# Kernel optimization log

Hardware: AMD Instinct MI355X
Metric: run time of the kernel (lower is better)

## Reference

```python
import jax, jax.numpy as jnp
import numpy as np

B, NP, NG = 4, 8192, 8192

def setup_inputs() -> dict:
    key = jax.random.key(0)
    k1, k2, k3 = jax.random.split(key, 3)
    pr_pts = jax.random.normal(k1, (B, NP, 3), dtype=jnp.float32)
    gt_pts = jax.random.normal(k2, (B, NG, 3), dtype=jnp.float32)
    gt_valid = jax.random.randint(k3, (B, NG), 0, 2) > 0
    return {"pr_pts": pr_pts, "gt_pts": gt_pts, "gt_valid": gt_valid}

def _sq_dists(a, b):
    # a: [B,N,3], b: [B,M,3] -> squared pairwise distances [B,N,M]
    a2 = jnp.sum(a * a, -1)  # [B,N]
    b2 = jnp.sum(b * b, -1)  # [B,M]
    ab = jnp.einsum('bnd,bmd->bnm', a, b)
    return a2[:, :, None] + b2[:, None, :] - 2.0 * ab

def reference(pr_pts, gt_pts, gt_valid):
    # Bidirectional Chamfer distance with gt validity mask.
    d2 = _sq_dists(pr_pts, gt_pts)  # [B,Np,Ng]
    # accuracy: for each predicted point, min squared dist to a VALID gt point
    d2_masked = jnp.where(gt_valid[:, None, :], d2, jnp.inf)
    acc_b = jnp.mean(jnp.min(d2_masked, axis=-1), axis=-1)  # [B]
    # completeness: for each valid gt point, min squared dist to any pred point
    min_over_pr = jnp.min(d2, axis=1)  # [B,Ng]
    valid_f = gt_valid.astype(min_over_pr.dtype)
    com_b = jnp.sum(min_over_pr * valid_f, axis=-1) / jnp.maximum(jnp.sum(valid_f, axis=-1), 1.0)
    loss_acc = jnp.mean(acc_b)
    loss_com = jnp.mean(com_b)
    loss_cd = loss_acc + loss_com
    # Sum((loss_acc,None),(loss_com,None),(loss_cd,None)) with scalar losses -> acc+com+cd
    return loss_acc + loss_com + loss_cd
```

## Files before the change

kernel.cpp:

```cpp
#include <hip/hip_runtime.h>

#define BB 4
#define NN 8192

typedef _Float16 f16;
typedef _Float16 f16x8 __attribute__((ext_vector_type(8)));
typedef float f32x16 __attribute__((ext_vector_type(16)));

#define SZ_PACK (BB * NN * 16)
#define OFF_PART_BYTES (4 * SZ_PACK * 2)
#define OFF_RES_BYTES (OFF_PART_BYTES + 16 * NN * 4)

__global__ __launch_bounds__(256) void k_init(
    const float* __restrict__ pr, const float* __restrict__ gt,
    const int* __restrict__ valid,
    f16* __restrict__ APR, f16* __restrict__ BGT,
    f16* __restrict__ AGT, f16* __restrict__ BPR,
    float* __restrict__ res) {
  int i = blockIdx.x * 256 + threadIdx.x;
  if (blockIdx.x == 0 && threadIdx.x < 16) res[threadIdx.x] = 0.0f;
  if (i >= BB * NN) return;
  float px = pr[3 * i], py = pr[3 * i + 1], pz = pr[3 * i + 2];
  float gx = gt[3 * i], gy = gt[3 * i + 1], gz = gt[3 * i + 2];
  int vld = valid[i] != 0;

  f16 phx = (f16)px, phy = (f16)py, phz = (f16)pz;
  f16 plx = (f16)(px - (float)phx), ply = (f16)(py - (float)phy), plz = (f16)(pz - (float)phz);
  float p2 = px * px + py * py + pz * pz;
  f16 p2h = (f16)p2, p2l = (f16)(p2 - (float)p2h);

  f16 ghx = (f16)gx, ghy = (f16)gy, ghz = (f16)gz;
  f16 glx = (f16)(gx - (float)ghx), gly = (f16)(gy - (float)ghy), glz = (f16)(gz - (float)ghz);
  float g2 = gx * gx + gy * gy + gz * gz;
  f16 g2h = (f16)g2, g2l = (f16)(g2 - (float)g2h);
  f16 g2hm = vld ? g2h : (f16)32768.0f;
  f16 g2lm = vld ? g2l : (f16)0.0f;

  const f16 one = (f16)1.0f, zero = (f16)0.0f;
  union Rec { f16 h[16]; uint4 u[2]; };

  Rec ra;
  ra.h[0] = (f16)(-2.f * (float)phx); ra.h[1] = (f16)(-2.f * (float)phy); ra.h[2] = (f16)(-2.f * (float)phz);
  ra.h[3] = ra.h[0]; ra.h[4] = ra.h[1]; ra.h[5] = ra.h[2];
  ra.h[6] = (f16)(-2.f * (float)plx); ra.h[7] = (f16)(-2.f * (float)ply); ra.h[8] = (f16)(-2.f * (float)plz);
  ra.h[9] = p2h; ra.h[10] = p2l; ra.h[11] = one; ra.h[12] = one;
  ra.h[13] = zero; ra.h[14] = zero; ra.h[15] = zero;
  ((uint4*)APR)[2 * i] = ra.u[0]; ((uint4*)APR)[2 * i + 1] = ra.u[1];

  Rec rb;
  rb.h[0] = phx; rb.h[1] = phy; rb.h[2] = phz;
  rb.h[3] = plx; rb.h[4] = ply; rb.h[5] = plz;
  rb.h[6] = phx; rb.h[7] = phy; rb.h[8] = phz;
  rb.h[9] = one; rb.h[10] = one; rb.h[11] = p2h; rb.h[12] = p2l;
  rb.h[13] = zero; rb.h[14] = zero; rb.h[15] = zero;
  ((uint4*)BPR)[2 * i] = rb.u[0]; ((uint4*)BPR)[2 * i + 1] = rb.u[1];

  Rec rc;
  rc.h[0] = (f16)(-2.f * (float)ghx); rc.h[1] = (f16)(-2.f * (float)ghy); rc.h[2] = (f16)(-2.f * (float)ghz);
  rc.h[3] = rc.h[0]; rc.h[4] = rc.h[1]; rc.h[5] = rc.h[2];
  rc.h[6] = (f16)(-2.f * (float)glx); rc.h[7] = (f16)(-2.f * (float)gly); rc.h[8] = (f16)(-2.f * (float)glz);
  rc.h[9] = g2h; rc.h[10] = g2l; rc.h[11] = one; rc.h[12] = one;
  rc.h[13] = zero; rc.h[14] = zero; rc.h[15] = zero;
  ((uint4*)AGT)[2 * i] = rc.u[0]; ((uint4*)AGT)[2 * i + 1] = rc.u[1];

  Rec rd;
  rd.h[0] = ghx; rd.h[1] = ghy; rd.h[2] = ghz;
  rd.h[3] = glx; rd.h[4] = gly; rd.h[5] = glz;
  rd.h[6] = ghx; rd.h[7] = ghy; rd.h[8] = ghz;
  rd.h[9] = one; rd.h[10] = one; rd.h[11] = g2hm; rd.h[12] = g2lm;
  rd.h[13] = zero; rd.h[14] = zero; rd.h[15] = zero;
  ((uint4*)BGT)[2 * i] = rd.u[0]; ((uint4*)BGT)[2 * i + 1] = rd.u[1];
}

__global__ __launch_bounds__(256, 4) void k_dist(
    const f16* __restrict__ APR, const f16* __restrict__ BGT,
    const f16* __restrict__ AGT, const f16* __restrict__ BPR,
    float* __restrict__ partial) {
  __shared__ f16 lds[2 * 1024 * 8];
  int id = blockIdx.x;
  int wgrow = id & 63;
  int half  = (id >> 6) & 1;
  int b     = (id >> 7) & 3;
  int p     = id >> 9;
  const f16* A  = p ? AGT : APR;
  const f16* Bv = p ? BPR : BGT;
  int tid = threadIdx.x;
  int wave = tid >> 6, lane = tid & 63;
  int nn = lane & 31, q = lane >> 5;

  const f16* Ab = A + ((size_t)b * NN + wgrow * 128 + wave * 32 + nn) * 16 + q * 8;
  f16x8 af = *(const f16x8*)Ab;

  f32x16 zc = {};
  f32x16 m;
#pragma unroll
  for (int i = 0; i < 16; ++i) m[i] = 1e38f;

  const uint4* gsrc = (const uint4*)(Bv + ((size_t)b * NN + half * 4096) * 16);
  uint4* ldsu = (uint4*)lds;
  const f16x8* lf = (const f16x8*)lds;

  for (int chunk = 0; chunk < 4; ++chunk) {
    const uint4* src = gsrc + (size_t)chunk * 2048;
#pragma unroll
    for (int k = 0; k < 8; ++k) {
      int u = tid + 256 * k;
      ldsu[(u & 1) * 1024 + (u >> 1)] = src[u];
    }
    __syncthreads();
    for (int t = 0; t < 32; t += 2) {
      f16x8 b0 = lf[q * 1024 + t * 32 + nn];
      f16x8 b1 = lf[q * 1024 + (t + 1) * 32 + nn];
      f32x16 d0 = __builtin_amdgcn_mfma_f32_32x32x16_f16(af, b0, zc, 0, 0, 0);
      f32x16 d1 = __builtin_amdgcn_mfma_f32_32x32x16_f16(af, b1, zc, 0, 0, 0);
#pragma unroll
      for (int i = 0; i < 16; ++i)
        m[i] = fminf(fminf(d0[i], d1[i]), m[i]);
    }
    __syncthreads();
  }

#pragma unroll
  for (int i = 0; i < 16; ++i) {
    float v = m[i];
    v = fminf(v, __shfl_xor(v, 1, 64));
    v = fminf(v, __shfl_xor(v, 2, 64));
    v = fminf(v, __shfl_xor(v, 4, 64));
    v = fminf(v, __shfl_xor(v, 8, 64));
    v = fminf(v, __shfl_xor(v, 16, 64));
    m[i] = fmaxf(v, 0.0f);
  }

  float* pb = partial + (((size_t)(p * 4 + b) * 2 + half) * NN) + wgrow * 128 + wave * 32;
#pragma unroll
  for (int reg = 0; reg < 16; ++reg) {
    int rit = (reg & 3) + 8 * (reg >> 2) + 4 * q;
    if ((lane & 31) == reg) pb[rit] = m[reg];
  }
}

__global__ __launch_bounds__(256) void k_red(
    const float* __restrict__ partial, const int* __restrict__ valid,
    float* __restrict__ res) {
  int g = blockIdx.x >> 3, seg = blockIdx.x & 7;
  int pp = g >> 2, bb = g & 3;
  int tid = threadIdx.x;
  const float* pb = partial + (size_t)g * 2 * NN;

  float sum = 0.0f, cnt = 0.0f;
#pragma unroll
  for (int k = 0; k < 4; ++k) {
    int r = seg * 1024 + tid + 256 * k;
    float v = fminf(pb[r], pb[NN + r]);
    if (pp == 0) {
      sum += v;
    } else {
      int vld = valid[bb * NN + r] != 0;
      sum += vld ? v : 0.0f;
      cnt += vld ? 1.0f : 0.0f;
    }
  }
  __shared__ float r1[256], r2[256];
  r1[tid] = sum; r2[tid] = cnt;
  __syncthreads();
  for (int off = 128; off > 0; off >>= 1) {
    if (tid < off) { r1[tid] += r1[tid + off]; r2[tid] += r2[tid + off]; }
    __syncthreads();
  }
  if (tid == 0) {
    if (pp == 0) {
      atomicAdd(&res[bb], r1[0]);
    } else {
      atomicAdd(&res[4 + bb], r1[0]);
      atomicAdd(&res[8 + bb], r2[0]);
    }
  }
}

__global__ void k_final(const float* __restrict__ res, float* __restrict__ out) {
  if (threadIdx.x == 0 && blockIdx.x == 0) {
    float a = 0.f, c = 0.f;
    for (int bb = 0; bb < 4; ++bb) {
      a += res[bb] / (float)NN;
      c += res[4 + bb] / fmaxf(res[8 + bb], 1.0f);
    }
    out[0] = 0.5f * (a + c);
  }
}

extern "C" void kernel_launch(void* const* d_in, const int* in_sizes, int n_in,
                              void* d_out, int out_size, void* d_ws, size_t ws_size,
                              hipStream_t stream) {
  const float* pr    = (const float*)d_in[0];
  const float* gt    = (const float*)d_in[1];
  const int*   valid = (const int*)d_in[2];

  f16* base = (f16*)d_ws;
  f16* APR = base;
  f16* BGT = base + SZ_PACK;
  f16* AGT = base + 2 * SZ_PACK;
  f16* BPR = base + 3 * SZ_PACK;
  float* partial = (float*)((char*)d_ws + OFF_PART_BYTES);
  float* res     = (float*)((char*)d_ws + OFF_RES_BYTES);

  k_init<<<(BB * NN) / 256, 256, 0, stream>>>(pr, gt, valid, APR, BGT, AGT, BPR, res);
  k_dist<<<1024, 256, 0, stream>>>(APR, BGT, AGT, BPR, partial);
  k_red<<<64, 256, 0, stream>>>(partial, valid, res);
  k_final<<<1, 64, 0, stream>>>(res, (float*)d_out);
}
```

Before: 88.78 us.

## Compute both Chamfer directions from one distance matrix with row and column mins

Instead of running the MFMA distance tile twice (pred→gt and gt→pred with swapped operands), each tile is computed once, and both its row minima and its column minima are reduced. Column minima are gathered across waves through shared memory and written as 32 per-row-block partials that the reduction kernel then folds. This halves the MFMA work and removes the packing of two operand arrays. The cost is extra VALU min reductions, cross-lane shuffles, LDS traffic and a larger partial buffer to reduce. Each wave now handles two A fragments, and B fragments are prefetched one step ahead.

```diff
diff --git a/kernel.cpp b/kernel.cpp
--- a/kernel.cpp
+++ b/kernel.cpp
@@ -8,15 +8,16 @@
 typedef float f32x16 __attribute__((ext_vector_type(16)));
 
 #define SZ_PACK (BB * NN * 16)
-#define OFF_PART_BYTES (4 * SZ_PACK * 2)
-#define OFF_RES_BYTES (OFF_PART_BYTES + 16 * NN * 4)
+#define OFF_PROW_BYTES (2 * SZ_PACK * 2)
+#define SZ_PROW (BB * 8 * NN)
+#define OFF_PCOL_BYTES (OFF_PROW_BYTES + SZ_PROW * 4)
+#define SZ_PCOL (BB * 32 * NN)
+#define OFF_RES_BYTES (OFF_PCOL_BYTES + SZ_PCOL * 4)
 
 __global__ __launch_bounds__(256) void k_init(
     const float* __restrict__ pr, const float* __restrict__ gt,
     const int* __restrict__ valid,
-    f16* __restrict__ APR, f16* __restrict__ BGT,
-    f16* __restrict__ AGT, f16* __restrict__ BPR,
-    float* __restrict__ res) {
+    f16* __restrict__ APR, f16* __restrict__ BGT, float* __restrict__ res) {
   int i = blockIdx.x * 256 + threadIdx.x;
   if (blockIdx.x == 0 && threadIdx.x < 16) res[threadIdx.x] = 0.0f;
   if (i >= BB * NN) return;
@@ -47,22 +48,6 @@
   ra.h[13] = zero; ra.h[14] = zero; ra.h[15] = zero;
   ((uint4*)APR)[2 * i] = ra.u[0]; ((uint4*)APR)[2 * i + 1] = ra.u[1];
 
-  Rec rb;
-  rb.h[0] = phx; rb.h[1] = phy; rb.h[2] = phz;
-  rb.h[3] = plx; rb.h[4] = ply; rb.h[5] = plz;
-  rb.h[6] = phx; rb.h[7] = phy; rb.h[8] = phz;
-  rb.h[9] = one; rb.h[10] = one; rb.h[11] = p2h; rb.h[12] = p2l;
-  rb.h[13] = zero; rb.h[14] = zero; rb.h[15] = zero;
-  ((uint4*)BPR)[2 * i] = rb.u[0]; ((uint4*)BPR)[2 * i + 1] = rb.u[1];
-
-  Rec rc;
-  rc.h[0] = (f16)(-2.f * (float)ghx); rc.h[1] = (f16)(-2.f * (float)ghy); rc.h[2] = (f16)(-2.f * (float)ghz);
-  rc.h[3] = rc.h[0]; rc.h[4] = rc.h[1]; rc.h[5] = rc.h[2];
-  rc.h[6] = (f16)(-2.f * (float)glx); rc.h[7] = (f16)(-2.f * (float)gly); rc.h[8] = (f16)(-2.f * (float)glz);
-  rc.h[9] = g2h; rc.h[10] = g2l; rc.h[11] = one; rc.h[12] = one;
-  rc.h[13] = zero; rc.h[14] = zero; rc.h[15] = zero;
-  ((uint4*)AGT)[2 * i] = rc.u[0]; ((uint4*)AGT)[2 * i + 1] = rc.u[1];
-
   Rec rd;
   rd.h[0] = ghx; rd.h[1] = ghy; rd.h[2] = ghz;
   rd.h[3] = glx; rd.h[4] = gly; rd.h[5] = glz;
@@ -72,105 +57,157 @@
   ((uint4*)BGT)[2 * i] = rd.u[0]; ((uint4*)BGT)[2 * i + 1] = rd.u[1];
 }
 
+__device__ __forceinline__ float min16(const f32x16& d) {
+  float v = fminf(fminf(d[0], d[1]), d[2]);
+  v = fminf(fminf(v, d[3]), d[4]);
+  v = fminf(fminf(v, d[5]), d[6]);
+  v = fminf(fminf(v, d[7]), d[8]);
+  v = fminf(fminf(v, d[9]), d[10]);
+  v = fminf(fminf(v, d[11]), d[12]);
+  v = fminf(fminf(v, d[13]), d[14]);
+  return fminf(v, d[15]);
+}
+
 __global__ __launch_bounds__(256, 4) void k_dist(
     const f16* __restrict__ APR, const f16* __restrict__ BGT,
-    const f16* __restrict__ AGT, const f16* __restrict__ BPR,
-    float* __restrict__ partial) {
-  __shared__ f16 lds[2 * 1024 * 8];
+    float* __restrict__ prow, float* __restrict__ pcol) {
+  __shared__ f16 ldsB[2 * 512 * 8];
+  __shared__ float colmin_s[4][512];
   int id = blockIdx.x;
-  int wgrow = id & 63;
-  int half  = (id >> 6) & 1;
-  int b     = (id >> 7) & 3;
-  int p     = id >> 9;
-  const f16* A  = p ? AGT : APR;
-  const f16* Bv = p ? BPR : BGT;
+  int wgrow  = id & 31;
+  int eighth = (id >> 5) & 7;
+  int b      = id >> 8;
   int tid = threadIdx.x;
   int wave = tid >> 6, lane = tid & 63;
   int nn = lane & 31, q = lane >> 5;
 
-  const f16* Ab = A + ((size_t)b * NN + wgrow * 128 + wave * 32 + nn) * 16 + q * 8;
-  f16x8 af = *(const f16x8*)Ab;
+  const f16* Ab = APR + ((size_t)b * NN + wgrow * 256 + wave * 64 + nn) * 16 + q * 8;
+  f16x8 af0 = *(const f16x8*)Ab;
+  f16x8 af1 = *(const f16x8*)(Ab + 32 * 16);
 
   f32x16 zc = {};
-  f32x16 m;
-#pragma unroll
-  for (int i = 0; i < 16; ++i) m[i] = 1e38f;
-
-  const uint4* gsrc = (const uint4*)(Bv + ((size_t)b * NN + half * 4096) * 16);
-  uint4* ldsu = (uint4*)lds;
-  const f16x8* lf = (const f16x8*)lds;
-
-  for (int chunk = 0; chunk < 4; ++chunk) {
-    const uint4* src = gsrc + (size_t)chunk * 2048;
-#pragma unroll
-    for (int k = 0; k < 8; ++k) {
+  f32x16 m0, m1;
+#pragma unroll
+  for (int i = 0; i < 16; ++i) { m0[i] = 1e38f; m1[i] = 1e38f; }
+
+  const uint4* gsrc = (const uint4*)(BGT + ((size_t)b * NN + eighth * 1024) * 16);
+  uint4* ldsu = (uint4*)ldsB;
+  const f16x8* lf = (const f16x8*)ldsB;
+
+  for (int chunk = 0; chunk < 2; ++chunk) {
+    const uint4* src = gsrc + chunk * 1024;
+#pragma unroll
+    for (int k = 0; k < 4; ++k) {
       int u = tid + 256 * k;
-      ldsu[(u & 1) * 1024 + (u >> 1)] = src[u];
-    }
-    __syncthreads();
-    for (int t = 0; t < 32; t += 2) {
-      f16x8 b0 = lf[q * 1024 + t * 32 + nn];
-      f16x8 b1 = lf[q * 1024 + (t + 1) * 32 + nn];
-      f32x16 d0 = __builtin_amdgcn_mfma_f32_32x32x16_f16(af, b0, zc, 0, 0, 0);
-      f32x16 d1 = __builtin_amdgcn_mfma_f32_32x32x16_f16(af, b1, zc, 0, 0, 0);
-#pragma unroll
-      for (int i = 0; i < 16; ++i)
-        m[i] = fminf(fminf(d0[i], d1[i]), m[i]);
-    }
-    __syncthreads();
+      ldsu[(u & 1) * 512 + (u >> 1)] = src[u];
+    }
+    __syncthreads();
+    f16x8 b0 = lf[q * 512 + 0 * 32 + nn];
+    f16x8 b1 = lf[q * 512 + 1 * 32 + nn];
+    for (int t = 0; t < 16; t += 2) {
+      int tn = (t + 2) & 15;
+      f16x8 nb0 = lf[q * 512 + tn * 32 + nn];
+      f16x8 nb1 = lf[q * 512 + (tn + 1) * 32 + nn];
+      f32x16 d0 = __builtin_amdgcn_mfma_f32_32x32x16_f16(af0, b0, zc, 0, 0, 0);
+      f32x16 d1 = __builtin_amdgcn_mfma_f32_32x32x16_f16(af0, b1, zc, 0, 0, 0);
+#pragma unroll
+      for (int i = 0; i < 16; ++i) m0[i] = fminf(fminf(d0[i], d1[i]), m0[i]);
+      float c00 = min16(d0), c01 = min16(d1);
+      f32x16 d2 = __builtin_amdgcn_mfma_f32_32x32x16_f16(af1, b0, zc, 0, 0, 0);
+      f32x16 d3 = __builtin_amdgcn_mfma_f32_32x32x16_f16(af1, b1, zc, 0, 0, 0);
+#pragma unroll
+      for (int i = 0; i < 16; ++i) m1[i] = fminf(fminf(d2[i], d3[i]), m1[i]);
+      float c0 = fminf(c00, min16(d2));
+      float c1 = fminf(c01, min16(d3));
+      c0 = fminf(c0, __shfl_xor(c0, 32, 64));
+      c1 = fminf(c1, __shfl_xor(c1, 32, 64));
+      if (q == 0) {
+        colmin_s[wave][t * 32 + nn] = c0;
+        colmin_s[wave][(t + 1) * 32 + nn] = c1;
+      }
+      b0 = nb0; b1 = nb1;
+    }
+    __syncthreads();
+    float* pc = pcol + ((size_t)b * 32 + wgrow) * NN + eighth * 1024 + chunk * 512;
+#pragma unroll
+    for (int e = 0; e < 2; ++e) {
+      int c = tid + 256 * e;
+      float v = fminf(fminf(colmin_s[0][c], colmin_s[1][c]),
+                      fminf(colmin_s[2][c], colmin_s[3][c]));
+      pc[c] = fmaxf(v, 0.0f);
+    }
   }
 
 #pragma unroll
   for (int i = 0; i < 16; ++i) {
-    float v = m[i];
+    float v = m0[i];
     v = fminf(v, __shfl_xor(v, 1, 64));
     v = fminf(v, __shfl_xor(v, 2, 64));
     v = fminf(v, __shfl_xor(v, 4, 64));
     v = fminf(v, __shfl_xor(v, 8, 64));
     v = fminf(v, __shfl_xor(v, 16, 64));
-    m[i] = fmaxf(v, 0.0f);
-  }
-
-  float* pb = partial + (((size_t)(p * 4 + b) * 2 + half) * NN) + wgrow * 128 + wave * 32;
+    m0[i] = fmaxf(v, 0.0f);
+    v = m1[i];
+    v = fminf(v, __shfl_xor(v, 1, 64));
+    v = fminf(v, __shfl_xor(v, 2, 64));
+    v = fminf(v, __shfl_xor(v, 4, 64));
+    v = fminf(v, __shfl_xor(v, 8, 64));
+    v = fminf(v, __shfl_xor(v, 16, 64));
+    m1[i] = fmaxf(v, 0.0f);
+  }
+  float* pb = prow + ((size_t)b * 8 + eighth) * NN + wgrow * 256 + wave * 64;
 #pragma unroll
   for (int reg = 0; reg < 16; ++reg) {
     int rit = (reg & 3) + 8 * (reg >> 2) + 4 * q;
-    if ((lane & 31) == reg) pb[rit] = m[reg];
+    if (nn == reg) { pb[rit] = m0[reg]; pb[32 + rit] = m1[reg]; }
   }
 }
 
 __global__ __launch_bounds__(256) void k_red(
-    const float* __restrict__ partial, const int* __restrict__ valid,
-    float* __restrict__ res) {
-  int g = blockIdx.x >> 3, seg = blockIdx.x & 7;
-  int pp = g >> 2, bb = g & 3;
-  int tid = threadIdx.x;
-  const float* pb = partial + (size_t)g * 2 * NN;
-
+    const float* __restrict__ prow, const float* __restrict__ pcol,
+    const int* __restrict__ valid, float* __restrict__ res) {
+  int bid = blockIdx.x, tid = threadIdx.x;
+  __shared__ float r1[256], r2[256];
   float sum = 0.0f, cnt = 0.0f;
-#pragma unroll
-  for (int k = 0; k < 4; ++k) {
-    int r = seg * 1024 + tid + 256 * k;
-    float v = fminf(pb[r], pb[NN + r]);
-    if (pp == 0) {
+  if (bid < 32) {
+    int bb = bid >> 3, seg = bid & 7;
+#pragma unroll
+    for (int k = 0; k < 4; ++k) {
+      int r = seg * 1024 + tid + 256 * k;
+      const float* p = prow + (size_t)bb * 8 * NN + r;
+      float v = p[0];
+#pragma unroll
+      for (int e = 1; e < 8; ++e) v = fminf(v, p[(size_t)e * NN]);
       sum += v;
-    } else {
-      int vld = valid[bb * NN + r] != 0;
+    }
+    r1[tid] = sum;
+    __syncthreads();
+    for (int off = 128; off > 0; off >>= 1) {
+      if (tid < off) r1[tid] += r1[tid + off];
+      __syncthreads();
+    }
+    if (tid == 0) atomicAdd(&res[bb], r1[0]);
+  } else {
+    int g = bid - 32;
+    int bb = g >> 4, seg = g & 15;
+#pragma unroll
+    for (int k = 0; k < 2; ++k) {
+      int j = seg * 512 + tid + 256 * k;
+      const float* p = pcol + (size_t)bb * 32 * NN + j;
+      float v = p[0];
+#pragma unroll
+      for (int w = 1; w < 32; ++w) v = fminf(v, p[(size_t)w * NN]);
+      int vld = valid[bb * NN + j] != 0;
       sum += vld ? v : 0.0f;
       cnt += vld ? 1.0f : 0.0f;
     }
-  }
-  __shared__ float r1[256], r2[256];
-  r1[tid] = sum; r2[tid] = cnt;
-  __syncthreads();
-  for (int off = 128; off > 0; off >>= 1) {
-    if (tid < off) { r1[tid] += r1[tid + off]; r2[tid] += r2[tid + off]; }
-    __syncthreads();
-  }
-  if (tid == 0) {
-    if (pp == 0) {
-      atomicAdd(&res[bb], r1[0]);
-    } else {
+    r1[tid] = sum; r2[tid] = cnt;
+    __syncthreads();
+    for (int off = 128; off > 0; off >>= 1) {
+      if (tid < off) { r1[tid] += r1[tid + off]; r2[tid] += r2[tid + off]; }
+      __syncthreads();
+    }
+    if (tid == 0) {
       atomicAdd(&res[4 + bb], r1[0]);
       atomicAdd(&res[8 + bb], r2[0]);
     }
@@ -198,13 +235,12 @@
   f16* base = (f16*)d_ws;
   f16* APR = base;
   f16* BGT = base + SZ_PACK;
-  f16* AGT = base + 2 * SZ_PACK;
-  f16* BPR = base + 3 * SZ_PACK;
-  float* partial = (float*)((char*)d_ws + OFF_PART_BYTES);
-  float* res     = (float*)((char*)d_ws + OFF_RES_BYTES);
-
-  k_init<<<(BB * NN) / 256, 256, 0, stream>>>(pr, gt, valid, APR, BGT, AGT, BPR, res);
-  k_dist<<<1024, 256, 0, stream>>>(APR, BGT, AGT, BPR, partial);
-  k_red<<<64, 256, 0, stream>>>(partial, valid, res);
+  float* prow = (float*)((char*)d_ws + OFF_PROW_BYTES);
+  float* pcol = (float*)((char*)d_ws + OFF_PCOL_BYTES);
+  float* res  = (float*)((char*)d_ws + OFF_RES_BYTES);
+
+  k_init<<<(BB * NN) / 256, 256, 0, stream>>>(pr, gt, valid, APR, BGT, res);
+  k_dist<<<1024, 256, 0, stream>>>(APR, BGT, prow, pcol);
+  k_red<<<96, 256, 0, stream>>>(prow, pcol, valid, res);
   k_final<<<1, 64, 0, stream>>>(res, (float*)d_out);
 }
```

Measured after the change: 87.81 us (median of 2 runs). Within noise of the previous version (-1.1%).
